# Kernel tuning notes

Measured on AMD Instinct MI355X. Metric: run time of the kernel, lower is better.

The kernel has to match this reference:

```python
import jax, jax.numpy as jnp
import numpy as np

B = 16384          # batch size
NNZ_PER = 32       # active features per position (pieces)
NNZ = B * NNZ_PER
FT_OUT = 512
F_BIG = 49152
F_SMALL = 768
MOD = 640


def setup_inputs() -> dict:
    key = jax.random.key(0)
    ks = jax.random.split(key, 8)
    rows = jnp.repeat(jnp.arange(NNZ // NNZ_PER, dtype=jnp.int64), NNZ_PER)
    stm_cols = jax.random.randint(ks[0], (NNZ,), 0, F_BIG, dtype=jnp.int64)
    nstm_cols = jax.random.randint(ks[1], (NNZ,), 0, F_BIG, dtype=jnp.int64)
    stm_indices = jnp.stack([rows, stm_cols])   # [2, nnz] COO (row, col)
    nstm_indices = jnp.stack([rows, nstm_cols])
    values = jnp.ones((NNZ,), dtype=jnp.float32)
    s = 0.01
    W_ft = jax.random.normal(ks[2], (FT_OUT, F_BIG), dtype=jnp.float32) * s
    b_ft = jax.random.normal(ks[3], (FT_OUT,), dtype=jnp.float32) * s
    W_fft = jax.random.normal(ks[4], (FT_OUT, F_SMALL), dtype=jnp.float32) * s
    b_fft = jax.random.normal(ks[5], (FT_OUT,), dtype=jnp.float32) * s
    W_out = jax.random.normal(ks[6], (1, FT_OUT * 2), dtype=jnp.float32) * s
    b_out = jax.random.normal(ks[7], (1,), dtype=jnp.float32) * s
    return {
        "stm_indices": stm_indices, "nstm_indices": nstm_indices,
        "values": values, "size": B,
        "W_ft": W_ft, "b_ft": b_ft, "W_fft": W_fft, "b_fft": b_fft,
        "W_out": W_out, "b_out": b_out,
    }


def _sparse_linear(indices, values, W, b, size, mod=None):
    # sparse [size, in] @ W.T + b, sparse given as COO (rows, cols, values).
    rows, cols = indices[0], indices[1]
    if mod is not None:
        # faithful to source: `% mod` applied to BOTH row and col indices
        rows = rows % mod
        cols = cols % mod
    contrib = values[:, None] * W.T[cols]            # [nnz, ft_out] gather
    acc = jax.ops.segment_sum(contrib, rows, num_segments=size)
    return acc + b


def reference(stm_indices, nstm_indices, values, size,
              W_ft, b_ft, W_fft, b_fft, W_out, b_out):
    stm_ft = (_sparse_linear(stm_indices, values, W_ft, b_ft, size)
              + _sparse_linear(stm_indices, values, W_fft, b_fft, size, MOD))
    nstm_ft = (_sparse_linear(nstm_indices, values, W_ft, b_ft, size)
               + _sparse_linear(nstm_indices, values, W_fft, b_fft, size, MOD))
    hidden = jnp.clip(jnp.concatenate([stm_ft, nstm_ft], axis=1), 0.0, 1.0)
    return jax.nn.sigmoid(hidden @ W_out.T + b_out)
```

## Files before the change

kernel.cpp:

```cpp
#include <hip/hip_runtime.h>
#include <math.h>

#define B_SZ    16384
#define NNZ_PER 32
#define NNZ     (B_SZ * NNZ_PER)
#define FT_OUT  512
#define F_BIG   49152
#define F_SMALL 768
#define MODV    640

#define TP_A     1536
#define TP_B     80
#define HISTB    (2 * MODV)
#define PREP_GRID (TP_A + TP_B + HISTB)

#define NSLICE  8
#define SL_F    64
#define MAIN_G  16
#define MAIN_GRID (NSLICE * (B_SZ / (4 * MAIN_G)))

#define FFT_SROWS 16
#define FFT_OQ    128
#define FFT_BLOCKS (2 * (MODV / FFT_SROWS) * (FT_OUT / FFT_OQ))

#define FP8_SCALE     256.0f
#define FP8_INV_SCALE 0.00390625f


typedef __attribute__((ext_vector_type(2))) float f32x2;

__device__ __forceinline__ float clip01(float x) {
    return fminf(fmaxf(x, 0.0f), 1.0f);
}

__device__ __forceinline__ unsigned long long gld2(unsigned long long base,
                                                   unsigned voff) {
    unsigned long long r;
    asm volatile("global_load_dwordx2 %0, %1, %2"
                 : "=v"(r) : "v"(voff), "s"(base));
    return r;
}

__device__ __forceinline__ void fma8_fp8(unsigned d0, unsigned d1, float v,
                                         float* a) {
    f32x2 p;
    p = __builtin_amdgcn_cvt_pk_f32_fp8(d0, false); a[0] += v * p.x; a[1] += v * p.y;
    p = __builtin_amdgcn_cvt_pk_f32_fp8(d0, true);  a[2] += v * p.x; a[3] += v * p.y;
    p = __builtin_amdgcn_cvt_pk_f32_fp8(d1, false); a[4] += v * p.x; a[5] += v * p.y;
    p = __builtin_amdgcn_cvt_pk_f32_fp8(d1, true);  a[6] += v * p.x; a[7] += v * p.y;
}

__global__ __launch_bounds__(256)
void prep_kernel(const float* __restrict__ W_ft, const float* __restrict__ W_fft,
                 const int* __restrict__ stm, const int* __restrict__ nstm,
                 const float* __restrict__ vals,
                 unsigned char* __restrict__ Wt, float* __restrict__ Wfft_t,
                 float* __restrict__ H) {
    __shared__ __align__(16) unsigned char smem[256 * 17 * 4];
    int b = blockIdx.x;
    int tid = threadIdx.x;
    if (b < TP_A) {
        unsigned (*tA32)[17] = (unsigned (*)[17])smem;
        int ct = b >> 1, ot = b & 1;
        int c0 = ct * 64, o0 = ot * 256;
        int orow = tid >> 4, c4 = (tid & 15) * 4;
#pragma unroll
        for (int it = 0; it < 16; it++) {
            int oo = orow + it * 16;
            float4 f = *(const float4*)(W_ft + (size_t)(o0 + oo) * F_BIG + c0 + c4);
            int r = 0;
            r = __builtin_amdgcn_cvt_pk_fp8_f32(f.x * FP8_SCALE, f.y * FP8_SCALE, r, false);
            r = __builtin_amdgcn_cvt_pk_fp8_f32(f.z * FP8_SCALE, f.w * FP8_SCALE, r, true);
            tA32[oo][c4 >> 2] = (unsigned)r;
        }
        __syncthreads();
        int cc = tid >> 2, fs = (tid & 3) * 16;
        int cw = cc >> 2, cb = (cc & 3) * 8;
#pragma unroll
        for (int ss = 0; ss < 4; ss++) {
            int ob = ss * 64 + fs;
            unsigned bw[4];
#pragma unroll
            for (int w = 0; w < 4; w++) {
                unsigned e0 = (tA32[ob + 4 * w + 0][cw] >> cb) & 0xffu;
                unsigned e1 = (tA32[ob + 4 * w + 1][cw] >> cb) & 0xffu;
                unsigned e2 = (tA32[ob + 4 * w + 2][cw] >> cb) & 0xffu;
                unsigned e3 = (tA32[ob + 4 * w + 3][cw] >> cb) & 0xffu;
                bw[w] = e0 | (e1 << 8) | (e2 << 16) | (e3 << 24);
            }
            int s = (o0 >> 6) + ss;
            unsigned char* dst = Wt + ((size_t)s * F_BIG + (c0 + cc)) * SL_F + fs;
            *(uint4*)dst = make_uint4(bw[0], bw[1], bw[2], bw[3]);
        }
    } else if (b < TP_A + TP_B) {
        float (*tB)[65] = (float (*)[65])smem;
        int b2 = b - TP_A;
        int nct = MODV / 64;
        int ot = b2 / nct, ct = b2 % nct;
        int c0 = ct * 64, o0 = ot * 64;
        int rr = tid >> 4, c4 = (tid & 15) * 4;
#pragma unroll
        for (int it = 0; it < 4; it++) {
            int oo = rr + it * 16;
            float4 f = *(const float4*)(W_fft + (size_t)(o0 + oo) * F_SMALL + c0 + c4);
            tB[oo][c4 + 0] = f.x; tB[oo][c4 + 1] = f.y;
            tB[oo][c4 + 2] = f.z; tB[oo][c4 + 3] = f.w;
        }
        __syncthreads();
#pragma unroll
        for (int it = 0; it < 4; it++) {
            int idx = tid + it * 256;
            int cc = idx >> 4, g = idx & 15;
            float4 v = make_float4(tB[g * 4 + 0][cc], tB[g * 4 + 1][cc],
                                   tB[g * 4 + 2][cc], tB[g * 4 + 3][cc]);
            *(float4*)(Wfft_t + (size_t)(c0 + cc) * FT_OUT + o0 + g * 4) = v;
        }
    } else {
        float* hrow = (float*)smem;
        int hb   = b - TP_A - TP_B;
        int side = (hb >= MODV) ? 1 : 0;
        int r    = hb - side * MODV;
        const int* cols = (side ? nstm : stm) + NNZ;
        for (int i = tid; i < MODV; i += 256) hrow[i] = 0.0f;
        __syncthreads();
        int nb  = (B_SZ - r + MODV - 1) / MODV;
        int tot = nb * NNZ_PER;
        for (int idx = tid; idx < tot; idx += 256) {
            int j = r * NNZ_PER + (idx >> 5) * (MODV * NNZ_PER) + (idx & 31);
            int c = cols[j] % MODV;
            atomicAdd(&hrow[c], vals[j]);
        }
        __syncthreads();
        float* dst = H + ((size_t)side * MODV + r) * MODV;
        for (int i = tid; i < MODV; i += 256) dst[i] = hrow[i];
    }
}

__global__ __launch_bounds__(256)
void fft_gemm(const float* __restrict__ H, const float* __restrict__ Wfft_t,
              float* __restrict__ acc) {
    __shared__ float hst[FFT_SROWS][MODV];
    int b = blockIdx.x;
    int tid = threadIdx.x;
    int side  = b / 160;
    int rem   = b % 160;
    int s0    = (rem >> 2) * FFT_SROWS;
    int oq    = rem & 3;
    int o     = oq * FFT_OQ + (tid & 127);
    int jh    = (tid >> 7) * 8;

    const float* Hs = H + ((size_t)side * MODV + s0) * MODV;
    for (int t = tid; t < FFT_SROWS * MODV; t += 256)
        ((float*)hst)[t] = Hs[t];
    __syncthreads();

    float a[8] = {0, 0, 0, 0, 0, 0, 0, 0};
    const float* wp = Wfft_t + o;
    for (int cc0 = 0; cc0 < MODV; cc0 += 8) {
        float w[8];
#pragma unroll
        for (int u = 0; u < 8; u++) w[u] = wp[(size_t)(cc0 + u) * FT_OUT];
#pragma unroll
        for (int u = 0; u < 8; u++) {
#pragma unroll
            for (int j = 0; j < 8; j++)
                a[j] += hst[jh + j][cc0 + u] * w[u];
        }
    }
    float* dst = acc + ((size_t)side * MODV + s0 + jh) * FT_OUT + o;
#pragma unroll
    for (int j = 0; j < 8; j++) dst[(size_t)j * FT_OUT] = a[j];
}

__global__ __launch_bounds__(256)
void main_slice(const int* __restrict__ stm, const int* __restrict__ nstm,
                const float* __restrict__ vals,
                const unsigned char* __restrict__ Wt,
                const float* __restrict__ b_ft, const float* __restrict__ b_fft,
                const float* __restrict__ fft_acc,
                const float* __restrict__ W_out, float* __restrict__ partial) {
    int bid = blockIdx.x;
    int slice = bid & 7;
    int rowbase = (bid >> 3) * (4 * MAIN_G);
    int tid = threadIdx.x;

    __shared__ __align__(16) unsigned s_ct[2][4][2][32];
    __shared__ __align__(16) float    s_vf[2][4][32];

    int wid = tid >> 6, lane = tid & 63;
    int q = lane >> 3, fp = lane & 7;

    unsigned long long base =
        (unsigned long long)(Wt + (size_t)slice * ((size_t)F_BIG * SL_F));
    unsigned fb = (unsigned)fp * 8u;

    int rS = tid >> 6, sideS = (tid >> 5) & 1, kS = tid & 31;
    int tkS = (kS & 7) * 4 + (kS >> 3);
    const int* arrS = sideS ? nstm : stm;
    int rV = (tid >> 5) & 3, kV = tid & 31;
    int tkV = (kV & 7) * 4 + (kV >> 3);

    bool b3 = (lane & 8) != 0, b4 = (lane & 16) != 0, b5 = (lane & 32) != 0;
    int f  = fp * 8 + (b3 ? 4 : 0) + (b4 ? 2 : 0) + (b5 ? 1 : 0);
    int fo = slice * SL_F + f;
    float bsum = b_ft[fo] + b_fft[fo];
    float wo0 = W_out[fo], wo1 = W_out[FT_OUT + fo];

    s_ct[0][rS][sideS][tkS] = (unsigned)arrS[NNZ + (rowbase + rS) * NNZ_PER + kS] << 6;
    s_vf[0][rV][tkV] = vals[(rowbase + rV) * NNZ_PER + kV] * FP8_INV_SCALE;
    __syncthreads();

    int cur = 0;
    for (int g = 0; g < MAIN_G; g++) {
        int row = rowbase + g * 4 + wid;
        uint4  cs0 = *(const uint4*)&s_ct[cur][wid][0][q * 4];
        uint4  cs1 = *(const uint4*)&s_ct[cur][wid][1][q * 4];
        float4 vf  = *(const float4*)&s_vf[cur][wid][q * 4];

        unsigned long long w00 = gld2(base, cs0.x + fb);
        unsigned long long w01 = gld2(base, cs0.y + fb);
        unsigned long long w02 = gld2(base, cs0.z + fb);
        unsigned long long w03 = gld2(base, cs0.w + fb);
        unsigned long long w10 = gld2(base, cs1.x + fb);
        unsigned long long w11 = gld2(base, cs1.y + fb);
        unsigned long long w12 = gld2(base, cs1.z + fb);
        unsigned long long w13 = gld2(base, cs1.w + fb);

        float a0[8] = {0, 0, 0, 0, 0, 0, 0, 0};
        float a1[8] = {0, 0, 0, 0, 0, 0, 0, 0};

        asm volatile("s_waitcnt vmcnt(0)" ::: "memory");
        __builtin_amdgcn_sched_barrier(0);
        fma8_fp8((unsigned)w00, (unsigned)(w00 >> 32), vf.x, a0);
        fma8_fp8((unsigned)w01, (unsigned)(w01 >> 32), vf.y, a0);
        fma8_fp8((unsigned)w02, (unsigned)(w02 >> 32), vf.z, a0);
        fma8_fp8((unsigned)w03, (unsigned)(w03 >> 32), vf.w, a0);
        fma8_fp8((unsigned)w10, (unsigned)(w10 >> 32), vf.x, a1);
        fma8_fp8((unsigned)w11, (unsigned)(w11 >> 32), vf.y, a1);
        fma8_fp8((unsigned)w12, (unsigned)(w12 >> 32), vf.z, a1);
        fma8_fp8((unsigned)w13, (unsigned)(w13 >> 32), vf.w, a1);

        unsigned nc = 0; float nv = 0.0f;
        if (g + 1 < MAIN_G) {
            int rn = rowbase + (g + 1) * 4;
            nc = (unsigned)arrS[NNZ + (rn + rS) * NNZ_PER + kS] << 6;
            nv = vals[(rn + rV) * NNZ_PER + kV] * FP8_INV_SCALE;
        }

        float s0[4], s1[4];
#pragma unroll
        for (int i = 0; i < 4; i++) {
            float k0 = b3 ? a0[i + 4] : a0[i], x0 = b3 ? a0[i] : a0[i + 4];
            float k1 = b3 ? a1[i + 4] : a1[i], x1 = b3 ? a1[i] : a1[i + 4];
            s0[i] = k0 + __shfl_xor(x0, 8, 64);
            s1[i] = k1 + __shfl_xor(x1, 8, 64);
        }
        float m0[2], m1[2];
#pragma unroll
        for (int j = 0; j < 2; j++) {
            float k0 = b4 ? s0[j + 2] : s0[j], x0 = b4 ? s0[j] : s0[j + 2];
            float k1 = b4 ? s1[j + 2] : s1[j], x1 = b4 ? s1[j] : s1[j + 2];
            m0[j] = k0 + __shfl_xor(x0, 16, 64);
            m1[j] = k1 + __shfl_xor(x1, 16, 64);
        }
        float r0 = (b5 ? m0[1] : m0[0]) + __shfl_xor(b5 ? m0[0] : m0[1], 32, 64);
        float r1 = (b5 ? m1[1] : m1[0]) + __shfl_xor(b5 ? m1[0] : m1[1], 32, 64);

        float fa0 = 0.0f, fa1 = 0.0f;
        if (row < MODV) {
            fa0 = fft_acc[(size_t)row * FT_OUT + fo];
            fa1 = fft_acc[(size_t)(MODV + row) * FT_OUT + fo];
        }
        float d = clip01(r0 + bsum + fa0) * wo0 + clip01(r1 + bsum + fa1) * wo1;
#pragma unroll
        for (int off = 32; off > 0; off >>= 1)
            d += __shfl_down(d, off, 64);
        if (lane == 0)
            partial[(size_t)slice * B_SZ + row] = d;

        if (g + 1 < MAIN_G) {
            int nb = cur ^ 1;
            s_ct[nb][rS][sideS][tkS] = nc;
            s_vf[nb][rV][tkV] = nv;
            __syncthreads();
            cur = nb;
        }
    }
}

__global__ __launch_bounds__(256)
void finish(const float* __restrict__ partial, const float* __restrict__ b_out,
            float* __restrict__ out) {
    int row = blockIdx.x * 256 + threadIdx.x;
    float s = b_out[0];
#pragma unroll
    for (int j = 0; j < NSLICE; j++)
        s += partial[(size_t)j * B_SZ + row];
    out[row] = 1.0f / (1.0f + expf(-s));
}

extern "C" void kernel_launch(void* const* d_in, const int* in_sizes, int n_in,
                              void* d_out, int out_size, void* d_ws, size_t ws_size,
                              hipStream_t stream) {
    const int*   stm   = (const int*)d_in[0];
    const int*   nstm  = (const int*)d_in[1];
    const float* vals  = (const float*)d_in[2];
    const float* W_ft  = (const float*)d_in[4];
    const float* b_ft  = (const float*)d_in[5];
    const float* W_fft = (const float*)d_in[6];
    const float* b_fft = (const float*)d_in[7];
    const float* W_out = (const float*)d_in[8];
    const float* b_out = (const float*)d_in[9];
    float* out = (float*)d_out;

    unsigned char* Wt_f8 = (unsigned char*)d_ws;
    float* Wfft_t  = (float*)(Wt_f8 + (size_t)F_BIG * FT_OUT);
    float* H       = Wfft_t + (size_t)MODV * FT_OUT;
    float* fft_acc = H + (size_t)2 * MODV * MODV;
    float* partial = fft_acc + (size_t)2 * MODV * FT_OUT;

    prep_kernel<<<PREP_GRID, 256, 0, stream>>>(W_ft, W_fft, stm, nstm, vals,
                                               Wt_f8, Wfft_t, H);
    fft_gemm<<<FFT_BLOCKS, 256, 0, stream>>>(H, Wfft_t, fft_acc);
    main_slice<<<MAIN_GRID, 256, 0, stream>>>(stm, nstm, vals, Wt_f8, b_ft, b_fft,
                                              fft_acc, W_out, partial);
    finish<<<B_SZ / 256, 256, 0, stream>>>(partial, b_out, out);
}
```

Before: 279.6 us.

## Split fft_gemm reduction dimension four ways and stagger main load waits

```diff
diff --git a/kernel.cpp b/kernel.cpp
--- a/kernel.cpp
+++ b/kernel.cpp
@@ -21,7 +21,10 @@
 
 #define FFT_SROWS 16
 #define FFT_OQ    128
-#define FFT_BLOCKS (2 * (MODV / FFT_SROWS) * (FT_OUT / FFT_OQ))
+#define FFT_CCQ   4
+#define FFT_CCL   (MODV / FFT_CCQ)
+#define FFT_BLOCKS (2 * (MODV / FFT_SROWS) * (FT_OUT / FFT_OQ) * FFT_CCQ)
+#define FFT_PS    ((size_t)2 * MODV * FT_OUT)
 
 #define FP8_SCALE     256.0f
 #define FP8_INV_SCALE 0.00390625f
@@ -139,24 +142,28 @@
 __global__ __launch_bounds__(256)
 void fft_gemm(const float* __restrict__ H, const float* __restrict__ Wfft_t,
               float* __restrict__ acc) {
-    __shared__ float hst[FFT_SROWS][MODV];
+    __shared__ float hst[FFT_SROWS][FFT_CCL];
     int b = blockIdx.x;
     int tid = threadIdx.x;
-    int side  = b / 160;
-    int rem   = b % 160;
-    int s0    = (rem >> 2) * FFT_SROWS;
-    int oq    = rem & 3;
-    int o     = oq * FFT_OQ + (tid & 127);
-    int jh    = (tid >> 7) * 8;
-
-    const float* Hs = H + ((size_t)side * MODV + s0) * MODV;
-    for (int t = tid; t < FFT_SROWS * MODV; t += 256)
-        ((float*)hst)[t] = Hs[t];
+    int ccq  = b & 3;
+    int oq   = (b >> 2) & 3;
+    int st   = (b >> 4) % (MODV / FFT_SROWS);
+    int side = b / (FFT_BLOCKS / 2);
+    int s0   = st * FFT_SROWS;
+    int cb   = ccq * FFT_CCL;
+    int o    = oq * FFT_OQ + (tid & 127);
+    int jh   = (tid >> 7) * 8;
+
+    const float* Hs = H + ((size_t)side * MODV + s0) * MODV + cb;
+    for (int t = tid; t < FFT_SROWS * FFT_CCL; t += 256) {
+        int r = t / FFT_CCL, c = t - r * FFT_CCL;
+        hst[r][c] = Hs[(size_t)r * MODV + c];
+    }
     __syncthreads();
 
     float a[8] = {0, 0, 0, 0, 0, 0, 0, 0};
-    const float* wp = Wfft_t + o;
-    for (int cc0 = 0; cc0 < MODV; cc0 += 8) {
+    const float* wp = Wfft_t + (size_t)cb * FT_OUT + o;
+    for (int cc0 = 0; cc0 < FFT_CCL; cc0 += 8) {
         float w[8];
 #pragma unroll
         for (int u = 0; u < 8; u++) w[u] = wp[(size_t)(cc0 + u) * FT_OUT];
@@ -167,7 +174,8 @@
                 a[j] += hst[jh + j][cc0 + u] * w[u];
         }
     }
-    float* dst = acc + ((size_t)side * MODV + s0 + jh) * FT_OUT + o;
+    float* dst = acc + (size_t)ccq * FFT_PS
+               + ((size_t)side * MODV + s0 + jh) * FT_OUT + o;
 #pragma unroll
     for (int j = 0; j < 8; j++) dst[(size_t)j * FT_OUT] = a[j];
 }
@@ -229,12 +237,15 @@
         float a0[8] = {0, 0, 0, 0, 0, 0, 0, 0};
         float a1[8] = {0, 0, 0, 0, 0, 0, 0, 0};
 
-        asm volatile("s_waitcnt vmcnt(0)" ::: "memory");
+        asm volatile("s_waitcnt vmcnt(4)" ::: "memory");
         __builtin_amdgcn_sched_barrier(0);
         fma8_fp8((unsigned)w00, (unsigned)(w00 >> 32), vf.x, a0);
         fma8_fp8((unsigned)w01, (unsigned)(w01 >> 32), vf.y, a0);
         fma8_fp8((unsigned)w02, (unsigned)(w02 >> 32), vf.z, a0);
         fma8_fp8((unsigned)w03, (unsigned)(w03 >> 32), vf.w, a0);
+
+        asm volatile("s_waitcnt vmcnt(0)" ::: "memory");
+        __builtin_amdgcn_sched_barrier(0);
         fma8_fp8((unsigned)w10, (unsigned)(w10 >> 32), vf.x, a1);
         fma8_fp8((unsigned)w11, (unsigned)(w11 >> 32), vf.y, a1);
         fma8_fp8((unsigned)w12, (unsigned)(w12 >> 32), vf.z, a1);
@@ -268,8 +279,10 @@
 
         float fa0 = 0.0f, fa1 = 0.0f;
         if (row < MODV) {
-            fa0 = fft_acc[(size_t)row * FT_OUT + fo];
-            fa1 = fft_acc[(size_t)(MODV + row) * FT_OUT + fo];
+            const float* p = fft_acc + (size_t)row * FT_OUT + fo;
+            const float* pq = fft_acc + (size_t)(MODV + row) * FT_OUT + fo;
+            fa0 = p[0] + p[FFT_PS] + p[2 * FFT_PS] + p[3 * FFT_PS];
+            fa1 = pq[0] + pq[FFT_PS] + pq[2 * FFT_PS] + pq[3 * FFT_PS];
         }
         float d = clip01(r0 + bsum + fa0) * wo0 + clip01(r1 + bsum + fa1) * wo1;
 #pragma unroll
@@ -317,7 +330,7 @@
     float* Wfft_t  = (float*)(Wt_f8 + (size_t)F_BIG * FT_OUT);
     float* H       = Wfft_t + (size_t)MODV * FT_OUT;
     float* fft_acc = H + (size_t)2 * MODV * MODV;
-    float* partial = fft_acc + (size_t)2 * MODV * FT_OUT;
+    float* partial = fft_acc + (size_t)FFT_CCQ * FFT_PS;
 
     prep_kernel<<<PREP_GRID, 256, 0, stream>>>(W_ft, W_fft, stm, nstm, vals,
                                                Wt_f8, Wfft_t, H);
```

After: 265.4 us. 1.05x faster.
